# Kernel tuning notes

Hardware: AMD Instinct MI355X
Metric: run time of the kernel (lower is better)

## Reference

```python
import jax, jax.numpy as jnp
import numpy as np

NUM_STEPS = 3
NUM_POINTS = 5
LENGTH = 1.0
MAXVAL = float(np.sinh(LENGTH))


def setup_inputs() -> dict:
    key = jax.random.key(0)
    k1, k2, k3 = jax.random.split(key, 3)
    data = jax.random.normal(k1, (64, 128, 64, 64), jnp.float32)
    # control tables: row 0 = values at knots, row 1 = tangents (Hermite)
    velocity = jnp.concatenate(
        [jnp.linspace(0.0, 1.0, NUM_POINTS)[None, :],
         jnp.full((1, NUM_POINTS), 2.0 * np.pi / NUM_POINTS)], axis=0).astype(jnp.float32)
    angles = jnp.concatenate(
        [jnp.linspace(0.0, 2.0 * np.pi, NUM_POINTS)[None, :],
         jnp.full((1, NUM_POINTS), 2.0 * np.pi / NUM_POINTS)], axis=0).astype(jnp.float32)
    channel_transform = jax.random.normal(k2, (1, 1), jnp.float32)
    spatio_transform = jax.random.normal(k3, (1, 1), jnp.float32)
    return {"data": data, "velocity": velocity, "angles": angles,
            "channel_transform": channel_transform, "spatio_transform": spatio_transform}


def _handler(x):
    # bucketize x into one of the NUM_POINTS-1 spline segments (unit-width knots)
    t = jnp.clip(x, 0.0, float(NUM_POINTS - 1))
    i0 = jnp.clip(jnp.floor(t).astype(jnp.int32), 0, NUM_POINTS - 2)
    u = t - i0.astype(x.dtype)
    return i0, u


def _hermite(table, i0, u):
    v, m = table[0], table[1]  # values, tangents at knots
    u2 = u * u
    u3 = u2 * u
    h00 = 2.0 * u3 - 3.0 * u2 + 1.0
    h10 = u3 - 2.0 * u2 + u
    h01 = -2.0 * u3 + 3.0 * u2
    h11 = u3 - u2
    return h00 * v[i0] + h10 * m[i0] + h01 * v[i0 + 1] + h11 * m[i0 + 1]


def reference(data, velocity, angles, channel_transform, spatio_transform):
    B, C, H, W = data.shape
    x = data * MAXVAL
    x = x.reshape(B, C, H * W).transpose(0, 2, 1)  # (B, HW, C)
    x = x * channel_transform[0, 0]                # (.., 1) @ (1, 1) == scalar mul
    step = LENGTH / NUM_STEPS
    for _ in range(NUM_STEPS):
        i0, u = _handler(x)
        vel = _hermite(velocity, i0, u)
        ang = _hermite(angles, i0, u)
        x = x + (vel * jnp.cos(ang) + x * vel * jnp.sin(ang)) * step
    x = x * spatio_transform[0, 0]
    x = x.transpose(0, 2, 1).reshape(B, C, H, W)
    return x / MAXVAL
```

## Files before the change

### kernel.cpp

```cpp
#include <hip/hip_runtime.h>


#define MAXVAL_F 1.1752011936438014f

typedef float nfloat4 __attribute__((ext_vector_type(4)));

constexpr int   TAB_K  = 512;
constexpr int   REP    = 16;
constexpr float TAB_L0 = -0.5f;
constexpr float TAB_HI = 4.5f;
constexpr float INV_H  = (float)(TAB_K - 1) / (TAB_HI - TAB_L0);
constexpr int   ITER   = 8;
constexpr int   BLK    = 256;
constexpr int   F4_PER_BLOCK = BLK * ITER;

__device__ __forceinline__ float eval_exact(float x,
    const float* __restrict__ vt, const float* __restrict__ at) {
#pragma unroll
  for (int k = 0; k < 3; ++k) {
    float t = fminf(fmaxf(x, 0.0f), 4.0f);
    int i0 = (int)t;
    if (i0 > 3) i0 = 3;
    float u  = t - (float)i0;
    float u2 = u * u, u3 = u2 * u;
    float h00 =  2.0f * u3 - 3.0f * u2 + 1.0f;
    float h10 =         u3 - 2.0f * u2 + u;
    float h01 = -2.0f * u3 + 3.0f * u2;
    float h11 =         u3 -        u2;
    float vel = h00 * vt[i0] + h10 * vt[5 + i0] + h01 * vt[i0 + 1] + h11 * vt[6 + i0];
    float ang = h00 * at[i0] + h10 * at[5 + i0] + h01 * at[i0 + 1] + h11 * at[6 + i0];
    float sn = sinf(ang);
    float cs = cosf(ang);
    x = x + (vel * cs + x * vel * sn) * (1.0f / 3.0f);
  }
  return x;
}

__global__ void build_table_kernel(const float* __restrict__ vt,
                                   const float* __restrict__ at,
                                   const float* __restrict__ stp,
                                   float* __restrict__ gtab) {
  int j = blockIdx.x * blockDim.x + threadIdx.x;
  if (j >= TAB_K) return;
  float sc = stp[0] * (1.0f / MAXVAL_F);
  float x  = TAB_L0 + (float)j / INV_H;
  gtab[j] = eval_exact(x, vt, at) * sc;
}

__device__ __forceinline__ void nt_store4(float4 o, float4* p) {
  nfloat4 v = {o.x, o.y, o.z, o.w};
  __builtin_nontemporal_store(v, (nfloat4*)p);
}

__device__ __forceinline__ float lerp_tab(float x, float C1, float C0, int lrep,
                                          const float* __restrict__ vrep) {
  float s  = fmaf(x, C1, C0);
  float fj = fminf(fmaxf(floorf(s), 0.0f), (float)(TAB_K - 2));
  float u  = s - fj;
  int   off = ((int)fj << 4) | lrep;
  float a0 = vrep[off];
  float a1 = vrep[off + REP];
  return fmaf(u, a1 - a0, a0);
}

__global__ __launch_bounds__(BLK, 4) void apply_map_kernel(
    const float4* __restrict__ in, float4* __restrict__ out,
    const float* __restrict__ gtab, const float* __restrict__ ctp, int nf4) {
  __shared__ float vrep[TAB_K * REP];
  {
#pragma unroll
    for (int k = 0; k < (TAB_K * REP) / BLK; ++k) {
      int i = (int)threadIdx.x + k * BLK;
      vrep[i] = gtab[i >> 4];
    }
  }
  float C1 = ctp[0] * (MAXVAL_F * INV_H);
  const float C0 = -TAB_L0 * INV_H;
  int lrep = (int)threadIdx.x & (REP - 1);
  __syncthreads();

  int base = (int)blockIdx.x * F4_PER_BLOCK + (int)threadIdx.x;

  if (base + (ITER - 1) * BLK < nf4) {
    float4 d[ITER];
#pragma unroll
    for (int k = 0; k < ITER; ++k) d[k] = in[base + k * BLK];
#pragma unroll
    for (int k = 0; k < ITER; ++k) {
      float4 o;
      o.x = lerp_tab(d[k].x, C1, C0, lrep, vrep);
      o.y = lerp_tab(d[k].y, C1, C0, lrep, vrep);
      o.z = lerp_tab(d[k].z, C1, C0, lrep, vrep);
      o.w = lerp_tab(d[k].w, C1, C0, lrep, vrep);
      nt_store4(o, &out[base + k * BLK]);
    }
  } else {
#pragma unroll
    for (int k = 0; k < ITER; ++k) {
      int idx = base + k * BLK;
      if (idx < nf4) {
        float4 d = in[idx];
        float4 o;
        o.x = lerp_tab(d.x, C1, C0, lrep, vrep);
        o.y = lerp_tab(d.y, C1, C0, lrep, vrep);
        o.z = lerp_tab(d.z, C1, C0, lrep, vrep);
        o.w = lerp_tab(d.w, C1, C0, lrep, vrep);
        nt_store4(o, &out[idx]);
      }
    }
  }
}

extern "C" void kernel_launch(void* const* d_in, const int* in_sizes, int n_in,
                              void* d_out, int out_size, void* d_ws, size_t ws_size,
                              hipStream_t stream) {
  const float* data = (const float*)d_in[0];
  const float* vel  = (const float*)d_in[1];
  const float* ang  = (const float*)d_in[2];
  const float* ct   = (const float*)d_in[3];
  const float* st   = (const float*)d_in[4];
  float*       outp = (float*)d_out;
  float*       gtab = (float*)d_ws;

  hipLaunchKernelGGL(build_table_kernel, dim3((TAB_K + 255) / 256), dim3(256), 0, stream,
                     vel, ang, st, gtab);

  int n   = in_sizes[0];
  int nf4 = n / 4;
  int blocks = (nf4 + F4_PER_BLOCK - 1) / F4_PER_BLOCK;
  hipLaunchKernelGGL(apply_map_kernel, dim3(blocks), dim3(BLK), 0, stream,
                     (const float4*)data, (float4*)outp, gtab, ct, nf4);
}
```

Measured before the change: 241.1 us.

## Double-buffer input chunks per block and halve LDS table replication

Each block now handles four chunks and software-pipelines them with two register buffers, issuing the next chunk's loads before processing the current one. The first loads are issued before the barrier so they overlap the shared-memory table fill. LDS replication drops from 16 to 8 copies and the occupancy hint rises to 8 blocks per CU. The intent is to hide memory latency in this bandwidth-bound streaming kernel, at the cost of fewer blocks, more registers and possibly more LDS bank conflicts.

Result: no change. 245.1 us (+1.7%).

```diff
diff --git a/kernel.cpp b/kernel.cpp
--- a/kernel.cpp
+++ b/kernel.cpp
@@ -6,13 +6,15 @@
 typedef float nfloat4 __attribute__((ext_vector_type(4)));
 
 constexpr int   TAB_K  = 512;
-constexpr int   REP    = 16;
+constexpr int   REP    = 8;
 constexpr float TAB_L0 = -0.5f;
 constexpr float TAB_HI = 4.5f;
 constexpr float INV_H  = (float)(TAB_K - 1) / (TAB_HI - TAB_L0);
-constexpr int   ITER   = 8;
+constexpr int   ITER   = 4;
 constexpr int   BLK    = 256;
-constexpr int   F4_PER_BLOCK = BLK * ITER;
+constexpr int   NCHUNK = 4;
+constexpr int   F4_PER_CHUNK = BLK * ITER;
+constexpr int   F4_PER_BLOCK = F4_PER_CHUNK * NCHUNK;
 
 __device__ __forceinline__ float eval_exact(float x,
     const float* __restrict__ vt, const float* __restrict__ at) {
@@ -57,13 +59,27 @@
   float s  = fmaf(x, C1, C0);
   float fj = fminf(fmaxf(floorf(s), 0.0f), (float)(TAB_K - 2));
   float u  = s - fj;
-  int   off = ((int)fj << 4) | lrep;
+  int   off = ((int)fj << 3) | lrep;
   float a0 = vrep[off];
   float a1 = vrep[off + REP];
   return fmaf(u, a1 - a0, a0);
 }
 
-__global__ __launch_bounds__(BLK, 4) void apply_map_kernel(
+__device__ __forceinline__ void proc_store(const float4* d, int cbase,
+    float4* __restrict__ out, float C1, float C0, int lrep,
+    const float* __restrict__ vrep) {
+#pragma unroll
+  for (int j = 0; j < ITER; ++j) {
+    float4 o;
+    o.x = lerp_tab(d[j].x, C1, C0, lrep, vrep);
+    o.y = lerp_tab(d[j].y, C1, C0, lrep, vrep);
+    o.z = lerp_tab(d[j].z, C1, C0, lrep, vrep);
+    o.w = lerp_tab(d[j].w, C1, C0, lrep, vrep);
+    nt_store4(o, &out[cbase + j * BLK]);
+  }
+}
+
+__global__ __launch_bounds__(BLK, 8) void apply_map_kernel(
     const float4* __restrict__ in, float4* __restrict__ out,
     const float* __restrict__ gtab, const float* __restrict__ ctp, int nf4) {
   __shared__ float vrep[TAB_K * REP];
@@ -71,41 +87,46 @@
 #pragma unroll
     for (int k = 0; k < (TAB_K * REP) / BLK; ++k) {
       int i = (int)threadIdx.x + k * BLK;
-      vrep[i] = gtab[i >> 4];
+      vrep[i] = gtab[i >> 3];
     }
   }
   float C1 = ctp[0] * (MAXVAL_F * INV_H);
   const float C0 = -TAB_L0 * INV_H;
   int lrep = (int)threadIdx.x & (REP - 1);
-  __syncthreads();
 
   int base = (int)blockIdx.x * F4_PER_BLOCK + (int)threadIdx.x;
 
-  if (base + (ITER - 1) * BLK < nf4) {
-    float4 d[ITER];
+  if ((int)blockIdx.x * F4_PER_BLOCK + F4_PER_BLOCK <= nf4) {
+    float4 dA[ITER], dB[ITER];
 #pragma unroll
-    for (int k = 0; k < ITER; ++k) d[k] = in[base + k * BLK];
+    for (int j = 0; j < ITER; ++j) dA[j] = in[base + j * BLK];
+    __syncthreads();
 #pragma unroll
-    for (int k = 0; k < ITER; ++k) {
-      float4 o;
-      o.x = lerp_tab(d[k].x, C1, C0, lrep, vrep);
-      o.y = lerp_tab(d[k].y, C1, C0, lrep, vrep);
-      o.z = lerp_tab(d[k].z, C1, C0, lrep, vrep);
-      o.w = lerp_tab(d[k].w, C1, C0, lrep, vrep);
-      nt_store4(o, &out[base + k * BLK]);
-    }
+    for (int j = 0; j < ITER; ++j) dB[j] = in[base + F4_PER_CHUNK + j * BLK];
+    proc_store(dA, base, out, C1, C0, lrep, vrep);
+#pragma unroll
+    for (int j = 0; j < ITER; ++j) dA[j] = in[base + 2 * F4_PER_CHUNK + j * BLK];
+    proc_store(dB, base + F4_PER_CHUNK, out, C1, C0, lrep, vrep);
+#pragma unroll
+    for (int j = 0; j < ITER; ++j) dB[j] = in[base + 3 * F4_PER_CHUNK + j * BLK];
+    proc_store(dA, base + 2 * F4_PER_CHUNK, out, C1, C0, lrep, vrep);
+    proc_store(dB, base + 3 * F4_PER_CHUNK, out, C1, C0, lrep, vrep);
   } else {
+    __syncthreads();
 #pragma unroll
-    for (int k = 0; k < ITER; ++k) {
-      int idx = base + k * BLK;
-      if (idx < nf4) {
-        float4 d = in[idx];
-        float4 o;
-        o.x = lerp_tab(d.x, C1, C0, lrep, vrep);
-        o.y = lerp_tab(d.y, C1, C0, lrep, vrep);
-        o.z = lerp_tab(d.z, C1, C0, lrep, vrep);
-        o.w = lerp_tab(d.w, C1, C0, lrep, vrep);
-        nt_store4(o, &out[idx]);
+    for (int c = 0; c < NCHUNK; ++c) {
+#pragma unroll
+      for (int j = 0; j < ITER; ++j) {
+        int idx = base + c * F4_PER_CHUNK + j * BLK;
+        if (idx < nf4) {
+          float4 d = in[idx];
+          float4 o;
+          o.x = lerp_tab(d.x, C1, C0, lrep, vrep);
+          o.y = lerp_tab(d.y, C1, C0, lrep, vrep);
+          o.z = lerp_tab(d.z, C1, C0, lrep, vrep);
+          o.w = lerp_tab(d.w, C1, C0, lrep, vrep);
+          nt_store4(o, &out[idx]);
+        }
       }
     }
   }
```
